# Kernel tuning notes

Hardware: AMD Instinct MI355X
Metric: run time of the kernel (lower is better)

The kernel has to match this reference:

```python
import jax, jax.numpy as jnp
import numpy as np

B, C, T = 16, 256, 1024
KERNEL_SPECS = [(3, 6), (5, 6), (9, 6)]
D = sum(o for _, o in KERNEL_SPECS)  # 18
TAU = 5.0
ALPHA = float(np.exp(-1.0 / TAU))
THRESHOLD = 0.01


def _dwconv(x, w, b, k):
    # x: (B,C,T), w: (C*out_per, 1, k) depthwise grouped conv, 'same' padding
    pad = (k - 1) // 2
    out = jax.lax.conv_general_dilated(
        x, w, window_strides=(1,), padding=[(pad, pad)],
        dimension_numbers=('NCH', 'OIH', 'NCH'), feature_group_count=C)
    return out + b[None, :, None]


def setup_inputs() -> dict:
    key = jax.random.key(0)
    ks = jax.random.split(key, 12)
    x = jax.random.normal(ks[0], (B, C, T), dtype=jnp.float32)
    params = {}
    for i, (k, op) in enumerate(KERNEL_SPECS):
        fan = k  # depthwise: 1 input channel per group
        bound = 1.0 / np.sqrt(fan)
        params[f'w{k}'] = jax.random.uniform(ks[1 + 2 * i], (C * op, 1, k), minval=-bound, maxval=bound, dtype=jnp.float32)
        params[f'b{k}'] = jax.random.uniform(ks[2 + 2 * i], (C * op,), minval=-bound, maxval=bound, dtype=jnp.float32)
    bound = 1.0 / np.sqrt(D)
    reduce_w = jax.random.uniform(ks[7], (C, D), minval=-bound, maxval=bound, dtype=jnp.float32)
    reduce_b = jax.random.uniform(ks[8], (C,), minval=-bound, maxval=bound, dtype=jnp.float32)
    latency_scale = jnp.asarray(5.0, dtype=jnp.float32)
    # xavier_uniform then zero diagonal
    g = np.sqrt(6.0 / (C + C))
    output_gates = jax.random.uniform(ks[9], (C, C), minval=-g, maxval=g, dtype=jnp.float32)
    output_gates = output_gates * (1.0 - jnp.eye(C, dtype=jnp.float32))
    filter_weights = 0.01 * jax.random.normal(ks[10], (C, C, D), dtype=jnp.float32)
    return dict(x=x, w3=params['w3'], b3=params['b3'], w5=params['w5'], b5=params['b5'],
                w9=params['w9'], b9=params['b9'], reduce_w=reduce_w, reduce_b=reduce_b,
                latency_scale=latency_scale, output_gates=output_gates,
                filter_weights=filter_weights)


def _lif_latency(drive):
    # drive: (B,C,T) -> latency (B,C); value T means 'no spike'
    Bc, Cc, Tc = drive.shape
    V0 = jnp.zeros((Bc, Cc), dtype=drive.dtype)
    fired0 = jnp.zeros((Bc, Cc), dtype=bool)
    lat0 = jnp.full((Bc, Cc), float(Tc), dtype=drive.dtype)

    def step(carry, inp):
        V, fired, lat = carry
        t, d_t = inp
        V = ALPHA * V + (1.0 - ALPHA) * d_t
        just = (V >= THRESHOLD) & (~fired)
        lat = jnp.where(just, t.astype(lat.dtype), lat)
        return (V, fired | just, lat), None

    ts = jnp.arange(Tc, dtype=jnp.float32)
    (_, _, lat), _ = jax.lax.scan(step, (V0, fired0, lat0), (ts, jnp.moveaxis(drive, 2, 0)))
    return lat


def reference(x, w3, b3, w5, b5, w9, b9, reduce_w, reduce_b,
              latency_scale, output_gates, filter_weights):
    ws = {3: (w3, b3), 5: (w5, b5), 9: (w9, b9)}
    outs = []
    for k, op in KERNEL_SPECS:
        w, b = ws[k]
        o = _dwconv(x, w, b, k)              # (B, C*op, T)
        outs.append(o.reshape(B, C, op, T))
    dendritic_drive = jnp.concatenate(outs, axis=2)  # (B, C, D, T)
    # grouped 1x1 reduce conv == per-channel weighted sum over D
    drive = jnp.einsum('bcdt,cd->bct', dendritic_drive, reduce_w) + reduce_b[None, :, None]
    true_lat = _lif_latency(drive)                    # (B, C)
    scale = jnp.maximum(latency_scale, 0.001)
    act = jnp.exp(-true_lat / scale)                  # (B, C)
    # padded kernel database (C, D, T)
    kp = jnp.zeros((C, D, T), dtype=x.dtype)
    off = 0
    for k, op in KERNEL_SPECS:
        w, _ = ws[k]
        kp = kp.at[:, off:off + op, :k].set(w.reshape(C, op, k))
        off += op
    coeff_base = output_gates[:, :, None] * filter_weights  # (Cj, Cc, D)
    recon = jnp.einsum('jcd,bc,cdt->bjt', coeff_base, act, kp)  # (B, C, T)
    return recon, x, true_lat, act
```

## Files before the change

### kernel.cpp

```cpp
#include <hip/hip_runtime.h>
#include <math.h>

#define Bb 16
#define Cc 256
#define Tt 1024

#define OFF_X   4194304
#define OFF_LAT 8388608
#define OFF_ACT 8392704

#define ALPHA_F 0.8187307530779818f
#define BETA_F  0.18126924692201815f
#define A16_F   0.04076220397836621f
#define THR_F   0.01f

__global__ __launch_bounds__(256) void k_main(
    const float* __restrict__ x,
    const float* __restrict__ w3, const float* __restrict__ b3,
    const float* __restrict__ w5, const float* __restrict__ b5,
    const float* __restrict__ w9, const float* __restrict__ b9,
    const float* __restrict__ rw, const float* __restrict__ rb,
    const float* __restrict__ ls, const float* __restrict__ og,
    const float* __restrict__ fw,
    float* __restrict__ H, float* __restrict__ out)
{
    const int bid = blockIdx.x;
    const int tid = threadIdx.x;

    if (bid >= 1024) {
        const int j = bid - 1024;
        const int c = tid;
        float h[9];
        #pragma unroll
        for (int t = 0; t < 9; ++t) h[t] = 0.f;
        const float g = og[j * 256 + c];
        const float* fwp = fw + (j * 256 + c) * 18;
        const float* w3p = w3 + c * 18;
        const float* w5p = w5 + c * 30;
        const float* w9p = w9 + c * 54;
        #pragma unroll
        for (int oi = 0; oi < 6; ++oi) {
            const float f3 = fwp[oi], f5 = fwp[6 + oi], f9 = fwp[12 + oi];
            #pragma unroll
            for (int t = 0; t < 3; ++t) h[t] = fmaf(f3, w3p[oi * 3 + t], h[t]);
            #pragma unroll
            for (int t = 0; t < 5; ++t) h[t] = fmaf(f5, w5p[oi * 5 + t], h[t]);
            #pragma unroll
            for (int t = 0; t < 9; ++t) h[t] = fmaf(f9, w9p[oi * 9 + t], h[t]);
        }
        #pragma unroll
        for (int t = 0; t < 9; ++t) H[(j * 9 + t) * 256 + c] = g * h[t];
        return;
    }

    const int lane = tid & 63;
    const int wid  = tid >> 6;
    const int row  = bid * 4 + wid;
    const int c    = row & 255;

    float el[9];
    #pragma unroll
    for (int r = 0; r < 9; ++r) el[r] = 0.f;
    float bl = 0.f;
    if (lane < 18) {
        const float r = rw[c * 18 + lane];
        if (lane < 6) {
            const int oi = lane;
            #pragma unroll
            for (int i = 0; i < 3; ++i) el[3 + i] = r * w3[c * 18 + oi * 3 + i];
            bl = r * b3[c * 6 + oi];
        } else if (lane < 12) {
            const int oi = lane - 6;
            #pragma unroll
            for (int i = 0; i < 5; ++i) el[2 + i] = r * w5[c * 30 + oi * 5 + i];
            bl = r * b5[c * 6 + oi];
        } else {
            const int oi = lane - 12;
            #pragma unroll
            for (int i = 0; i < 9; ++i) el[i] = r * w9[c * 54 + oi * 9 + i];
            bl = r * b9[c * 6 + oi];
        }
    }
    #pragma unroll
    for (int o = 1; o < 64; o <<= 1) {
        #pragma unroll
        for (int r = 0; r < 9; ++r) el[r] += __shfl_xor(el[r], o);
        bl += __shfl_xor(bl, o);
    }
    float e[9];
    #pragma unroll
    for (int r = 0; r < 9; ++r) e[r] = el[r];
    const float be = bl + rb[c];

    const float* xrow  = x + (size_t)row * Tt;
    const float4* xrow4 = reinterpret_cast<const float4*>(xrow);

    const int s = lane * 16;
    float xr[24];
    #pragma unroll
    for (int q = 0; q < 6; ++q) {
        const int t0 = s - 4 + 4 * q;
        float4 v = make_float4(0.f, 0.f, 0.f, 0.f);
        if (t0 >= 0 && t0 < Tt) v = xrow4[t0 >> 2];
        xr[q * 4 + 0] = v.x; xr[q * 4 + 1] = v.y;
        xr[q * 4 + 2] = v.z; xr[q * 4 + 3] = v.w;
    }

    float d[16];
    #pragma unroll
    for (int i = 0; i < 16; ++i) {
        float acc = be;
        #pragma unroll
        for (int r = 0; r < 9; ++r) acc = fmaf(e[r], xr[i + r], acc);
        d[i] = acc;
    }

    float Bl = 0.f;
    #pragma unroll
    for (int i = 0; i < 16; ++i) Bl = fmaf(ALPHA_F, Bl, BETA_F * d[i]);

    float Av = A16_F, Bv = Bl;
    #pragma unroll
    for (int o = 1; o < 64; o <<= 1) {
        const float Ap = __shfl_up(Av, (unsigned)o);
        const float Bp = __shfl_up(Bv, (unsigned)o);
        if (lane >= o) { Bv = fmaf(Av, Bp, Bv); Av = Av * Ap; }
    }
    float Vin = __shfl_up(Bv, 1u);
    if (lane == 0) Vin = 0.f;

    int local = -1;
    float V = Vin;
    #pragma unroll
    for (int i = 0; i < 16; ++i) {
        V = fmaf(ALPHA_F, V, BETA_F * d[i]);
        if (local < 0 && V >= THR_F) local = i;
    }
    const unsigned long long m = __ballot(local >= 0);
    float latf = 1024.f;
    if (m) {
        const int fl = __ffsll((unsigned long long)m) - 1;
        const int li = __shfl(local, fl);
        latf = (float)(fl * 16 + li);
    }
    const float scale = fmaxf(ls[0], 0.001f);
    const float act = expf(-latf / scale);

    float4* ox4 = reinterpret_cast<float4*>(out + OFF_X) + (size_t)row * 256;
    #pragma unroll
    for (int q = 0; q < 4; ++q) ox4[lane + 64 * q] = xrow4[lane + 64 * q];

    if (lane == 0) {
        out[OFF_LAT + row] = latf;
        out[OFF_ACT + row] = act;
    }
}

__global__ __launch_bounds__(256) void k_recon(
    const float* __restrict__ H, const float* __restrict__ actp,
    float* __restrict__ out)
{
    const int tid = threadIdx.x;
    const int bid = blockIdx.x;
    const int b = bid >> 8, j = bid & 255;

    const float a = actp[b * 256 + tid];
    float p[9];
    #pragma unroll
    for (int t = 0; t < 9; ++t) p[t] = a * H[(j * 9 + t) * 256 + tid];

    #pragma unroll
    for (int t = 0; t < 9; ++t) {
        #pragma unroll
        for (int o = 32; o > 0; o >>= 1) p[t] += __shfl_xor(p[t], o);
    }

    __shared__ float red[4][12];
    __shared__ float rs[12];
    const int lane = tid & 63, wid = tid >> 6;
    if (lane == 0) {
        #pragma unroll
        for (int t = 0; t < 9; ++t) red[wid][t] = p[t];
    }
    __syncthreads();
    if (tid < 9) rs[tid] = red[0][tid] + red[1][tid] + red[2][tid] + red[3][tid];
    __syncthreads();

    float4 v = make_float4(0.f, 0.f, 0.f, 0.f);
    if (tid == 0)      v = make_float4(rs[0], rs[1], rs[2], rs[3]);
    else if (tid == 1) v = make_float4(rs[4], rs[5], rs[6], rs[7]);
    else if (tid == 2) v = make_float4(rs[8], 0.f, 0.f, 0.f);
    reinterpret_cast<float4*>(out)[(size_t)bid * 256 + tid] = v;
}

extern "C" void kernel_launch(void* const* d_in, const int* in_sizes, int n_in,
                              void* d_out, int out_size, void* d_ws, size_t ws_size,
                              hipStream_t stream) {
    const float* x  = (const float*)d_in[0];
    const float* w3 = (const float*)d_in[1];
    const float* b3 = (const float*)d_in[2];
    const float* w5 = (const float*)d_in[3];
    const float* b5 = (const float*)d_in[4];
    const float* w9 = (const float*)d_in[5];
    const float* b9 = (const float*)d_in[6];
    const float* rw = (const float*)d_in[7];
    const float* rb = (const float*)d_in[8];
    const float* ls = (const float*)d_in[9];
    const float* og = (const float*)d_in[10];
    const float* fw = (const float*)d_in[11];
    float* out = (float*)d_out;

    float* H = (float*)d_ws;

    k_main<<<dim3(1280), dim3(256), 0, stream>>>(x, w3, b3, w5, b5, w9, b9,
                                                 rw, rb, ls, og, fw, H, out);
    k_recon<<<dim3(4096), dim3(256), 0, stream>>>(H, out + OFF_ACT, out);
}
```

Before: 113.2 us.

## Fuse reconstruction into main kernel with atomic accumulation of recon taps

Merges the latency/activation kernel and the reconstruction kernel into one launch. Each block handles four channels of one batch, computes their activations, then every thread (one output channel j) builds the filter taps for those four channels and adds its contribution to recon with atomic adds. A memset zeroes the recon region beforehand. The intent is to drop the H workspace round trip and the separate recon kernel, which wrote the full zero-padded recon tensor. The costs are redundant recomputation of the taps per batch (16x the filter_weights reads), heavy atomic contention on 9 floats per (b,j), and a memset of the whole recon buffer.

New measurement: 219.5 us. 93.9% more time.

```diff
diff --git a/kernel.cpp b/kernel.cpp
--- a/kernel.cpp
+++ b/kernel.cpp
@@ -14,7 +14,7 @@
 #define A16_F   0.04076220397836621f
 #define THR_F   0.01f
 
-__global__ __launch_bounds__(256) void k_main(
+__global__ __launch_bounds__(256) void k_fused(
     const float* __restrict__ x,
     const float* __restrict__ w3, const float* __restrict__ b3,
     const float* __restrict__ w5, const float* __restrict__ b5,
@@ -22,175 +22,160 @@
     const float* __restrict__ rw, const float* __restrict__ rb,
     const float* __restrict__ ls, const float* __restrict__ og,
     const float* __restrict__ fw,
-    float* __restrict__ H, float* __restrict__ out)
+    float* __restrict__ out)
 {
-    const int bid = blockIdx.x;
-    const int tid = threadIdx.x;
-
-    if (bid >= 1024) {
-        const int j = bid - 1024;
-        const int c = tid;
-        float h[9];
-        #pragma unroll
-        for (int t = 0; t < 9; ++t) h[t] = 0.f;
-        const float g = og[j * 256 + c];
-        const float* fwp = fw + (j * 256 + c) * 18;
-        const float* w3p = w3 + c * 18;
-        const float* w5p = w5 + c * 30;
-        const float* w9p = w9 + c * 54;
-        #pragma unroll
-        for (int oi = 0; oi < 6; ++oi) {
-            const float f3 = fwp[oi], f5 = fwp[6 + oi], f9 = fwp[12 + oi];
-            #pragma unroll
-            for (int t = 0; t < 3; ++t) h[t] = fmaf(f3, w3p[oi * 3 + t], h[t]);
-            #pragma unroll
-            for (int t = 0; t < 5; ++t) h[t] = fmaf(f5, w5p[oi * 5 + t], h[t]);
-            #pragma unroll
-            for (int t = 0; t < 9; ++t) h[t] = fmaf(f9, w9p[oi * 9 + t], h[t]);
-        }
-        #pragma unroll
-        for (int t = 0; t < 9; ++t) H[(j * 9 + t) * 256 + c] = g * h[t];
-        return;
-    }
-
+    const int bid  = blockIdx.x;
+    const int tid  = threadIdx.x;
     const int lane = tid & 63;
     const int wid  = tid >> 6;
-    const int row  = bid * 4 + wid;
-    const int c    = row & 255;
-
-    float el[9];
-    #pragma unroll
-    for (int r = 0; r < 9; ++r) el[r] = 0.f;
-    float bl = 0.f;
-    if (lane < 18) {
-        const float r = rw[c * 18 + lane];
-        if (lane < 6) {
-            const int oi = lane;
-            #pragma unroll
-            for (int i = 0; i < 3; ++i) el[3 + i] = r * w3[c * 18 + oi * 3 + i];
-            bl = r * b3[c * 6 + oi];
-        } else if (lane < 12) {
-            const int oi = lane - 6;
-            #pragma unroll
-            for (int i = 0; i < 5; ++i) el[2 + i] = r * w5[c * 30 + oi * 5 + i];
-            bl = r * b5[c * 6 + oi];
-        } else {
-            const int oi = lane - 12;
-            #pragma unroll
-            for (int i = 0; i < 9; ++i) el[i] = r * w9[c * 54 + oi * 9 + i];
-            bl = r * b9[c * 6 + oi];
+    const int b    = bid >> 6;
+    const int c0   = (bid & 63) << 2;
+
+    __shared__ float w3s[4][18];
+    __shared__ float w5s[4][30];
+    __shared__ float w9s[4][54];
+    __shared__ float act_s[4];
+
+    if (tid < 72)  w3s[tid / 18][tid % 18] = w3[(c0 + tid / 18) * 18 + tid % 18];
+    if (tid < 120) w5s[tid / 30][tid % 30] = w5[(c0 + tid / 30) * 30 + tid % 30];
+    if (tid < 216) w9s[tid / 54][tid % 54] = w9[(c0 + tid / 54) * 54 + tid % 54];
+
+    {
+        const int row = bid * 4 + wid;
+        const int c   = row & 255;
+
+        float el[9];
+        #pragma unroll
+        for (int r = 0; r < 9; ++r) el[r] = 0.f;
+        float bl = 0.f;
+        if (lane < 18) {
+            const float r = rw[c * 18 + lane];
+            if (lane < 6) {
+                const int oi = lane;
+                #pragma unroll
+                for (int i = 0; i < 3; ++i) el[3 + i] = r * w3[c * 18 + oi * 3 + i];
+                bl = r * b3[c * 6 + oi];
+            } else if (lane < 12) {
+                const int oi = lane - 6;
+                #pragma unroll
+                for (int i = 0; i < 5; ++i) el[2 + i] = r * w5[c * 30 + oi * 5 + i];
+                bl = r * b5[c * 6 + oi];
+            } else {
+                const int oi = lane - 12;
+                #pragma unroll
+                for (int i = 0; i < 9; ++i) el[i] = r * w9[c * 54 + oi * 9 + i];
+                bl = r * b9[c * 6 + oi];
+            }
+        }
+        #pragma unroll
+        for (int o = 1; o < 64; o <<= 1) {
+            #pragma unroll
+            for (int r = 0; r < 9; ++r) el[r] += __shfl_xor(el[r], o);
+            bl += __shfl_xor(bl, o);
+        }
+        const float be = bl + rb[c];
+
+        const float* xrow   = x + (size_t)row * Tt;
+        const float4* xrow4 = reinterpret_cast<const float4*>(xrow);
+
+        const int s = lane * 16;
+        float xr[24];
+        #pragma unroll
+        for (int q = 0; q < 6; ++q) {
+            const int t0 = s - 4 + 4 * q;
+            float4 v = make_float4(0.f, 0.f, 0.f, 0.f);
+            if (t0 >= 0 && t0 < Tt) v = xrow4[t0 >> 2];
+            xr[q * 4 + 0] = v.x; xr[q * 4 + 1] = v.y;
+            xr[q * 4 + 2] = v.z; xr[q * 4 + 3] = v.w;
+        }
+
+        float d[16];
+        #pragma unroll
+        for (int i = 0; i < 16; ++i) {
+            float acc = be;
+            #pragma unroll
+            for (int r = 0; r < 9; ++r) acc = fmaf(el[r], xr[i + r], acc);
+            d[i] = acc;
+        }
+
+        float Bl = 0.f;
+        #pragma unroll
+        for (int i = 0; i < 16; ++i) Bl = fmaf(ALPHA_F, Bl, BETA_F * d[i]);
+
+        float Av = A16_F, Bv = Bl;
+        #pragma unroll
+        for (int o = 1; o < 64; o <<= 1) {
+            const float Ap = __shfl_up(Av, (unsigned)o);
+            const float Bp = __shfl_up(Bv, (unsigned)o);
+            if (lane >= o) { Bv = fmaf(Av, Bp, Bv); Av = Av * Ap; }
+        }
+        float Vin = __shfl_up(Bv, 1u);
+        if (lane == 0) Vin = 0.f;
+
+        int local = -1;
+        float V = Vin;
+        #pragma unroll
+        for (int i = 0; i < 16; ++i) {
+            V = fmaf(ALPHA_F, V, BETA_F * d[i]);
+            if (local < 0 && V >= THR_F) local = i;
+        }
+        const unsigned long long m = __ballot(local >= 0);
+        float latf = 1024.f;
+        if (m) {
+            const int fl = __ffsll((unsigned long long)m) - 1;
+            const int li = __shfl(local, fl);
+            latf = (float)(fl * 16 + li);
+        }
+        const float scale = fmaxf(ls[0], 0.001f);
+        const float act = expf(-latf / scale);
+
+        float4* ox4 = reinterpret_cast<float4*>(out + OFF_X) + (size_t)row * 256;
+        #pragma unroll
+        for (int q = 0; q < 4; ++q) ox4[lane + 64 * q] = xrow4[lane + 64 * q];
+
+        if (lane == 0) {
+            out[OFF_LAT + row] = latf;
+            out[OFF_ACT + row] = act;
+            act_s[wid] = act;
         }
     }
-    #pragma unroll
-    for (int o = 1; o < 64; o <<= 1) {
-        #pragma unroll
-        for (int r = 0; r < 9; ++r) el[r] += __shfl_xor(el[r], o);
-        bl += __shfl_xor(bl, o);
+
+    __syncthreads();
+
+    {
+        const int j = tid;
+        const float4 ogv = *reinterpret_cast<const float4*>(og + j * 256 + c0);
+        const float ogf[4] = { ogv.x, ogv.y, ogv.z, ogv.w };
+
+        float acc[9];
+        #pragma unroll
+        for (int t = 0; t < 9; ++t) acc[t] = 0.f;
+
+        #pragma unroll
+        for (int ci = 0; ci < 4; ++ci) {
+            const float sgl = act_s[ci] * ogf[ci];
+            const float* fwp = fw + (size_t)((j * 256) + c0 + ci) * 18;
+            float h[9];
+            #pragma unroll
+            for (int t = 0; t < 9; ++t) h[t] = 0.f;
+            #pragma unroll
+            for (int oi = 0; oi < 6; ++oi) {
+                const float f3 = fwp[oi], f5 = fwp[6 + oi], f9 = fwp[12 + oi];
+                #pragma unroll
+                for (int t = 0; t < 3; ++t) h[t] = fmaf(f3, w3s[ci][oi * 3 + t], h[t]);
+                #pragma unroll
+                for (int t = 0; t < 5; ++t) h[t] = fmaf(f5, w5s[ci][oi * 5 + t], h[t]);
+                #pragma unroll
+                for (int t = 0; t < 9; ++t) h[t] = fmaf(f9, w9s[ci][oi * 9 + t], h[t]);
+            }
+            #pragma unroll
+            for (int t = 0; t < 9; ++t) acc[t] = fmaf(sgl, h[t], acc[t]);
+        }
+
+        float* op = out + (size_t)(b * 256 + j) * 1024;
+        #pragma unroll
+        for (int t = 0; t < 9; ++t) unsafeAtomicAdd(op + t, acc[t]);
     }
-    float e[9];
-    #pragma unroll
-    for (int r = 0; r < 9; ++r) e[r] = el[r];
-    const float be = bl + rb[c];
-
-    const float* xrow  = x + (size_t)row * Tt;
-    const float4* xrow4 = reinterpret_cast<const float4*>(xrow);
-
-    const int s = lane * 16;
-    float xr[24];
-    #pragma unroll
-    for (int q = 0; q < 6; ++q) {
-        const int t0 = s - 4 + 4 * q;
-        float4 v = make_float4(0.f, 0.f, 0.f, 0.f);
-        if (t0 >= 0 && t0 < Tt) v = xrow4[t0 >> 2];
-        xr[q * 4 + 0] = v.x; xr[q * 4 + 1] = v.y;
-        xr[q * 4 + 2] = v.z; xr[q * 4 + 3] = v.w;
-    }
-
-    float d[16];
-    #pragma unroll
-    for (int i = 0; i < 16; ++i) {
-        float acc = be;
-        #pragma unroll
-        for (int r = 0; r < 9; ++r) acc = fmaf(e[r], xr[i + r], acc);
-        d[i] = acc;
-    }
-
-    float Bl = 0.f;
-    #pragma unroll
-    for (int i = 0; i < 16; ++i) Bl = fmaf(ALPHA_F, Bl, BETA_F * d[i]);
-
-    float Av = A16_F, Bv = Bl;
-    #pragma unroll
-    for (int o = 1; o < 64; o <<= 1) {
-        const float Ap = __shfl_up(Av, (unsigned)o);
-        const float Bp = __shfl_up(Bv, (unsigned)o);
-        if (lane >= o) { Bv = fmaf(Av, Bp, Bv); Av = Av * Ap; }
-    }
-    float Vin = __shfl_up(Bv, 1u);
-    if (lane == 0) Vin = 0.f;
-
-    int local = -1;
-    float V = Vin;
-    #pragma unroll
-    for (int i = 0; i < 16; ++i) {
-        V = fmaf(ALPHA_F, V, BETA_F * d[i]);
-        if (local < 0 && V >= THR_F) local = i;
-    }
-    const unsigned long long m = __ballot(local >= 0);
-    float latf = 1024.f;
-    if (m) {
-        const int fl = __ffsll((unsigned long long)m) - 1;
-        const int li = __shfl(local, fl);
-        latf = (float)(fl * 16 + li);
-    }
-    const float scale = fmaxf(ls[0], 0.001f);
-    const float act = expf(-latf / scale);
-
-    float4* ox4 = reinterpret_cast<float4*>(out + OFF_X) + (size_t)row * 256;
-    #pragma unroll
-    for (int q = 0; q < 4; ++q) ox4[lane + 64 * q] = xrow4[lane + 64 * q];
-
-    if (lane == 0) {
-        out[OFF_LAT + row] = latf;
-        out[OFF_ACT + row] = act;
-    }
-}
-
-__global__ __launch_bounds__(256) void k_recon(
-    const float* __restrict__ H, const float* __restrict__ actp,
-    float* __restrict__ out)
-{
-    const int tid = threadIdx.x;
-    const int bid = blockIdx.x;
-    const int b = bid >> 8, j = bid & 255;
-
-    const float a = actp[b * 256 + tid];
-    float p[9];
-    #pragma unroll
-    for (int t = 0; t < 9; ++t) p[t] = a * H[(j * 9 + t) * 256 + tid];
-
-    #pragma unroll
-    for (int t = 0; t < 9; ++t) {
-        #pragma unroll
-        for (int o = 32; o > 0; o >>= 1) p[t] += __shfl_xor(p[t], o);
-    }
-
-    __shared__ float red[4][12];
-    __shared__ float rs[12];
-    const int lane = tid & 63, wid = tid >> 6;
-    if (lane == 0) {
-        #pragma unroll
-        for (int t = 0; t < 9; ++t) red[wid][t] = p[t];
-    }
-    __syncthreads();
-    if (tid < 9) rs[tid] = red[0][tid] + red[1][tid] + red[2][tid] + red[3][tid];
-    __syncthreads();
-
-    float4 v = make_float4(0.f, 0.f, 0.f, 0.f);
-    if (tid == 0)      v = make_float4(rs[0], rs[1], rs[2], rs[3]);
-    else if (tid == 1) v = make_float4(rs[4], rs[5], rs[6], rs[7]);
-    else if (tid == 2) v = make_float4(rs[8], 0.f, 0.f, 0.f);
-    reinterpret_cast<float4*>(out)[(size_t)bid * 256 + tid] = v;
 }
 
 extern "C" void kernel_launch(void* const* d_in, const int* in_sizes, int n_in,
@@ -210,9 +195,8 @@
     const float* fw = (const float*)d_in[11];
     float* out = (float*)d_out;
 
-    float* H = (float*)d_ws;
-
-    k_main<<<dim3(1280), dim3(256), 0, stream>>>(x, w3, b3, w5, b5, w9, b9,
-                                                 rw, rb, ls, og, fw, H, out);
-    k_recon<<<dim3(4096), dim3(256), 0, stream>>>(H, out + OFF_ACT, out);
+    hipMemsetAsync(out, 0, (size_t)OFF_X * sizeof(float), stream);
+
+    k_fused<<<dim3(1024), dim3(256), 0, stream>>>(x, w3, b3, w5, b5, w9, b9,
+                                                  rw, rb, ls, og, fw, out);
 }
```
